# Optimization experiments

Measured on AMD Instinct MI355X. Metric: run time of the kernel, lower is better.

## Reference

```python
import jax, jax.numpy as jnp
import numpy as np
import math

VOCAB = 256
EMBED = 1024
HEADS = 16
MAX_SEQ = 1024
B, S = 4, 1024
EPS = 1e-5


def setup_inputs() -> dict:
    key = jax.random.key(0)
    ks = jax.random.split(key, 10)
    x = jax.random.randint(ks[0], (B, S), 0, VOCAB)
    token_embedding = jax.random.normal(ks[1], (VOCAB, EMBED), dtype=jnp.float32)
    # positional phase buffer: pos * (1/10000**(dim/E)) * pi
    pos = jnp.arange(MAX_SEQ, dtype=jnp.float32)[:, None]
    dim = jnp.arange(EMBED, dtype=jnp.float32)[None, :]
    freq = 1.0 / (10000.0 ** (dim / EMBED))
    pos_phase = pos * freq * math.pi  # [MAX_SEQ, EMBED]
    hd = EMBED // HEADS
    q_rot = jax.random.uniform(ks[2], (HEADS, hd), minval=-math.pi, maxval=math.pi)
    k_rot = jax.random.uniform(ks[3], (HEADS, hd), minval=-math.pi, maxval=math.pi)
    v_rot = jax.random.uniform(ks[4], (HEADS, hd), minval=-math.pi, maxval=math.pi)
    # orthogonal-ish init for ff_real via QR
    a = jax.random.normal(ks[5], (EMBED, EMBED), dtype=jnp.float32)
    ff_real, _ = jnp.linalg.qr(a)
    ff_imag = jax.random.uniform(ks[6], (EMBED, EMBED), minval=-0.01, maxval=0.01)
    lim = 1.0 / math.sqrt(EMBED)
    ro_real_w = jax.random.uniform(ks[7], (VOCAB, EMBED), minval=-lim, maxval=lim)
    ro_real_b = jnp.zeros((VOCAB,), dtype=jnp.float32)
    ro_imag_w = jax.random.uniform(ks[8], (VOCAB, EMBED), minval=-lim, maxval=lim)
    ro_imag_b = jnp.zeros((VOCAB,), dtype=jnp.float32)
    return {
        "x": x,
        "token_embedding": token_embedding,
        "pos_phase": pos_phase,
        "q_rot": q_rot,
        "k_rot": k_rot,
        "v_rot": v_rot,
        "ff_real": ff_real,
        "ff_imag": ff_imag,
        "ro_real_w": ro_real_w,
        "ro_real_b": ro_real_b,
        "ro_imag_w": ro_imag_w,
        "ro_imag_b": ro_imag_b,
    }


def complex_norm(z):
    mag = jnp.abs(z)
    mean_mag = jnp.mean(mag, axis=-1, keepdims=True)
    std_mag = jnp.std(mag, axis=-1, keepdims=True, ddof=1)  # torch std is unbiased
    norm_mag = (mag - mean_mag) / (std_mag + EPS)
    scale = jnp.tanh(norm_mag) / (mag + EPS)
    return z * scale.astype(jnp.complex64)


def reference(x, token_embedding, pos_phase, q_rot, k_rot, v_rot,
              ff_real, ff_imag, ro_real_w, ro_real_b, ro_imag_w, ro_imag_b):
    b, s = x.shape
    h, hd = q_rot.shape
    mag = jnp.tanh(token_embedding[x])                       # [B,S,E]
    state = mag.astype(jnp.complex64) * jnp.exp(1j * pos_phase[:s].astype(jnp.complex64))[None]
    sh = state.reshape(b, s, h, hd)                          # [B,S,H,hd]
    q = sh * jnp.exp(1j * q_rot.astype(jnp.complex64))
    k = sh * jnp.exp(1j * k_rot.astype(jnp.complex64))
    v = sh * jnp.exp(1j * v_rot.astype(jnp.complex64))
    # complex QK^H interference -> take real part as logits
    interference = jnp.einsum('bqhd,bkhd->bhqk', q, jnp.conj(k))
    attn_logits = interference.real / math.sqrt(hd)
    causal = jnp.tril(jnp.ones((s, s), dtype=bool))
    attn_logits = jnp.where(causal[None, None], attn_logits, -jnp.inf)
    attn_weights = jax.nn.softmax(attn_logits * 8.0, axis=-1)  # [B,H,S,S]
    attn_out = jnp.einsum('bhqk,bkhd->bqhd', attn_weights.astype(jnp.complex64), v)
    attn_out = attn_out.reshape(b, s, h * hd)
    state = state + attn_out
    ff = ff_real.astype(jnp.complex64) + 1j * ff_imag.astype(jnp.complex64)
    state = state @ ff
    state = complex_norm(state)
    return state.real @ ro_real_w.T + ro_real_b + state.imag @ ro_imag_w.T + ro_imag_b
```

## Files before the change

### kernel.cpp

```cpp
#include <hip/hip_runtime.h>
#include <math.h>

#define B_ 4
#define S_ 1024
#define E_ 1024
#define H_ 16
#define V_ 256

typedef _Float16 h8 __attribute__((ext_vector_type(8)));
typedef _Float16 h4 __attribute__((ext_vector_type(4)));
typedef float f4x __attribute__((ext_vector_type(4)));

__device__ __forceinline__ void gload16(const void* g, void* l) {
  __builtin_amdgcn_global_load_lds((const __attribute__((address_space(1))) void*)g,
                                   (__attribute__((address_space(3))) void*)l, 16, 0, 0);
}

#define MFMA32F16(a, b, c) __builtin_amdgcn_mfma_f32_16x16x32_f16(a, b, c, 0, 0, 0)

#if defined(__has_builtin)
#if __has_builtin(__builtin_amdgcn_mfma_f32_16x16x16f16)
#define MFMA16F16(a, b, c) __builtin_amdgcn_mfma_f32_16x16x16f16(a, b, c, 0, 0, 0)
#endif
#endif
#ifndef MFMA16F16
__device__ __forceinline__ f4x mfma16f16_asm(h4 a, h4 b, f4x c) {
  asm volatile("v_mfma_f32_16x16x16_f16 %0, %1, %2, %0" : "+v"(c) : "v"(a), "v"(b));
  return c;
}
#define MFMA16F16(a, b, c) mfma16f16_asm(a, b, c)
#endif

__global__ void rot_kernel(const float* __restrict__ qr, const float* __restrict__ kr,
                           const float* __restrict__ vr, float* __restrict__ tabs) {
  int i = blockIdx.x * blockDim.x + threadIdx.x;
  if (i >= 3 * 1024) return;
  int which = i >> 10;
  int j = i & 1023;
  const float* src = which == 0 ? qr : (which == 1 ? kr : vr);
  float s, c;
  sincosf(src[j], &s, &c);
  tabs[which * 2048 + j] = c;
  tabs[which * 2048 + 1024 + j] = s;
}

__global__ __launch_bounds__(256) void embed_qkv_kernel(
    const int* __restrict__ x, const float* __restrict__ te,
    const float* __restrict__ pp, const float* __restrict__ tabs,
    float* __restrict__ sr, float* __restrict__ si,
    unsigned short* __restrict__ Kd, unsigned short* __restrict__ Vd) {
  __shared__ unsigned short Kl2[4096];
  __shared__ unsigned short Vl2[4096];
  const int kt2 = blockIdx.x;
  const int bh = blockIdx.y;
  const int b = bh >> 4, h = bh & 15;
  const int tid = threadIdx.x;
  const float* qc = tabs + h * 64;
  const float* qs = tabs + 1024 + h * 64;
  const float* kc = tabs + 2048 + h * 64;
  const float* ks = tabs + 3072 + h * 64;
  #pragma unroll
  for (int p = 0; p < 8; ++p) {
    int id = p * 256 + tid;
    int sl = id >> 6;
    int dd = id & 63;
    int s = kt2 * 32 + sl;
    int e = h * 64 + dd;
    int tok = x[b * 1024 + s];
    float mm = tanhf(te[tok * 1024 + e]);
    float sn, cs;
    sincosf(pp[s * 1024 + e], &sn, &cs);
    float re = mm * cs, im = mm * sn;
    size_t g = ((size_t)(b * 1024 + s)) * 1024 + e;
    sr[g] = re;
    si[g] = im;
    float cq = qc[dd], sq = qs[dd], ck = kc[dd], sk = ks[dd];
    float cd = cq * ck + sq * sk;
    float sd = sq * ck - cq * sk;
    float kr = re * cd + im * sd;
    float ki = im * cd - re * sd;
    int t = sl >> 4, key = sl & 15;
    int c0 = dd, c1 = 64 + dd;
    #define KOFF(c) (t * 2048 + ((((c) >> 5) * 4 + (((c) >> 3) & 3)) * 16 + key) * 8 + ((c) & 7))
    *(_Float16*)&Kl2[KOFF(c0)] = (_Float16)kr;
    *(_Float16*)&Kl2[KOFF(c1)] = (_Float16)ki;
    #undef KOFF
    int kgk = key >> 2, jk = key & 3;
    #define VOFF(d) (t * 2048 + ((((d) >> 4) * 4 + kgk) * 16 + ((d) & 15)) * 4 + jk)
    *(_Float16*)&Vl2[VOFF(dd)] = (_Float16)re;
    *(_Float16*)&Vl2[VOFF(64 + dd)] = (_Float16)im;
    #undef VOFF
  }
  __syncthreads();
  unsigned short* kdst = Kd + ((size_t)(bh * 64 + kt2 * 2)) * 2048;
  unsigned short* vdst = Vd + ((size_t)(bh * 64 + kt2 * 2)) * 2048;
  #pragma unroll
  for (int p = 0; p < 2; ++p) {
    int c = p * 256 + tid;
    ((int4*)kdst)[c] = ((const int4*)Kl2)[c];
    ((int4*)vdst)[c] = ((const int4*)Vl2)[c];
  }
}

__global__ __launch_bounds__(256, 4) void attn_mfma_kernel(
    const float* __restrict__ sr, const float* __restrict__ si,
    const unsigned short* __restrict__ Kd, const unsigned short* __restrict__ Vd,
    const float* __restrict__ tabs,
    unsigned short* __restrict__ Af) {
  __shared__ __align__(16) unsigned short Klds[2][4096];
  __shared__ __align__(16) unsigned short Vlds[2][4096];
  const int flat = blockIdx.x;
  const int low = flat & 7, rest = flat >> 3;
  const int a = rest >> 3;
  const int bh = ((rest & 7) << 3) | low;
  const int b = bh >> 4, h = bh & 15;
  const int tid = threadIdx.x, lane = tid & 63, wid = tid >> 6;
  const int cl = lane & 15, kg = lane >> 4;
  const int atile = (wid >> 1) ? (31 - a) : a;
  const int qw0 = atile * 32 + (wid & 1) * 16;

  h8 qf[4];
  {
    int q = qw0 + cl;
    const float* srow = sr + ((size_t)(b * 1024 + q)) * 1024 + h * 64;
    const float* irow = si + ((size_t)(b * 1024 + q)) * 1024 + h * 64;
    #pragma unroll
    for (int ksx = 0; ksx < 4; ++ksx) {
      int f0 = ksx * 32 + kg * 8;
      const float* src = (f0 < 64) ? (srow + f0) : (irow + (f0 - 64));
      float4 v0 = *(const float4*)src;
      float4 v1 = *(const float4*)(src + 4);
      qf[ksx][0] = (_Float16)v0.x; qf[ksx][1] = (_Float16)v0.y;
      qf[ksx][2] = (_Float16)v0.z; qf[ksx][3] = (_Float16)v0.w;
      qf[ksx][4] = (_Float16)v1.x; qf[ksx][5] = (_Float16)v1.y;
      qf[ksx][6] = (_Float16)v1.z; qf[ksx][7] = (_Float16)v1.w;
    }
  }

  f4x acc[8] = {};
  float m_ = -1e30f, l_ = 0.f;
  const int np = 32 - a;
  const int wqmax = qw0 + 15;
  const int qcol = qw0 + cl;

  const unsigned short* kstream = Kd + ((size_t)(bh * 64)) * 2048;
  const unsigned short* vstream = Vd + ((size_t)(bh * 64)) * 2048;

  #define STAGE_PAIR(buf, P)                                                    \
    {                                                                           \
      const unsigned short* kb = kstream + (size_t)(P) * 4096;                  \
      const unsigned short* vb = vstream + (size_t)(P) * 4096;                  \
      _Pragma("unroll")                                                         \
      for (int r = 0; r < 2; ++r) {                                             \
        int off = r * 256 + wid * 64;                                           \
        gload16(kb + (size_t)(off + lane) * 8, &Klds[buf][off * 8]);            \
        gload16(vb + (size_t)(off + lane) * 8, &Vlds[buf][off * 8]);            \
      }                                                                         \
    }

  STAGE_PAIR(0, 0)
  __syncthreads();

  for (int p = 0; p < np; ++p) {
    const int cur = p & 1;
    if (p + 1 < np) STAGE_PAIR(cur ^ 1, p + 1)
    const int k0a = p * 32;
    if (k0a <= wqmax) {
      __builtin_amdgcn_s_setprio(1);
      f4x sca = {}, scb = {};
      #pragma unroll
      for (int ksx = 0; ksx < 4; ++ksx) {
        h8 ka = *(const h8*)&Klds[cur][ksx * 512 + lane * 8];
        sca = MFMA32F16(ka, qf[ksx], sca);
      }
      #pragma unroll
      for (int ksx = 0; ksx < 4; ++ksx) {
        h8 kb = *(const h8*)&Klds[cur][2048 + ksx * 512 + lane * 8];
        scb = MFMA32F16(kb, qf[ksx], scb);
      }
      __builtin_amdgcn_s_setprio(0);
      if (k0a + 31 > qw0) {
        #pragma unroll
        for (int r = 0; r < 4; ++r) {
          if (k0a + kg * 4 + r > qcol)      sca[r] = -1e30f;
          if (k0a + 16 + kg * 4 + r > qcol) scb[r] = -1e30f;
        }
      }
      float mx = fmaxf(fmaxf(fmaxf(sca[0], sca[1]), fmaxf(sca[2], sca[3])),
                       fmaxf(fmaxf(scb[0], scb[1]), fmaxf(scb[2], scb[3])));
      mx = fmaxf(mx, __shfl_xor(mx, 16, 64));
      mx = fmaxf(mx, __shfl_xor(mx, 32, 64));
      if (!__all(mx <= m_ + 8.0f)) {
        float mn = fmaxf(m_, mx);
        float corr = __expf(m_ - mn);
        #pragma unroll
        for (int mt = 0; mt < 8; ++mt) acc[mt] *= corr;
        l_ *= corr;
        m_ = mn;
      }
      float pa0 = __expf(sca[0] - m_), pa1 = __expf(sca[1] - m_);
      float pa2 = __expf(sca[2] - m_), pa3 = __expf(sca[3] - m_);
      float pb0 = __expf(scb[0] - m_), pb1 = __expf(scb[1] - m_);
      float pb2 = __expf(scb[2] - m_), pb3 = __expf(scb[3] - m_);
      float s0 = ((pa0 + pa1) + (pa2 + pa3)) + ((pb0 + pb1) + (pb2 + pb3));
      s0 += __shfl_xor(s0, 16, 64);
      s0 += __shfl_xor(s0, 32, 64);
      l_ += s0;
      h4 pba, pbb;
      pba[0] = (_Float16)pa0; pba[1] = (_Float16)pa1;
      pba[2] = (_Float16)pa2; pba[3] = (_Float16)pa3;
      pbb[0] = (_Float16)pb0; pbb[1] = (_Float16)pb1;
      pbb[2] = (_Float16)pb2; pbb[3] = (_Float16)pb3;
      __builtin_amdgcn_s_setprio(1);
      #pragma unroll
      for (int mt = 0; mt < 8; ++mt) {
        h4 va = *(const h4*)&Vlds[cur][mt * 256 + lane * 4];
        acc[mt] = MFMA16F16(va, pba, acc[mt]);
      }
      #pragma unroll
      for (int mt = 0; mt < 8; ++mt) {
        h4 vb = *(const h4*)&Vlds[cur][2048 + mt * 256 + lane * 4];
        acc[mt] = MFMA16F16(vb, pbb, acc[mt]);
      }
      __builtin_amdgcn_s_setprio(0);
    }
    __syncthreads();
  }
  #undef STAGE_PAIR
  {
    float linv = 1.0f / l_;
    int q = qw0 + cl;
    size_t mrow = (size_t)(b * 1024 + q);
    size_t obase = mrow * 1024 + h * 64;
    size_t abase = mrow * 2048 + h * 64;
    #pragma unroll
    for (int mt = 0; mt < 4; ++mt) {
      int d0 = mt * 16 + kg * 4;
      float4 s_r = *(const float4*)&sr[obase + d0];
      float4 s_i = *(const float4*)&si[obase + d0];
      float srv[4] = {s_r.x, s_r.y, s_r.z, s_r.w};
      float siv[4] = {s_i.x, s_i.y, s_i.z, s_i.w};
      h4 hr, hi;
      #pragma unroll
      for (int r = 0; r < 4; ++r) {
        int d = d0 + r;
        float orv = acc[mt][r] * linv;
        float oiv = acc[mt + 4][r] * linv;
        float c = tabs[4096 + h * 64 + d], s = tabs[5120 + h * 64 + d];
        hr[r] = (_Float16)(orv * c - oiv * s + srv[r]);
        hi[r] = (_Float16)(orv * s + oiv * c + siv[r]);
      }
      *(h4*)&Af[abase + d0]        = hr;
      *(h4*)&Af[abase + 1024 + d0] = hi;
    }
  }
}

__global__ void split_b_kernel(const float* __restrict__ fr, const float* __restrict__ fi,
                               unsigned short* __restrict__ Bt) {
  __shared__ float tile[32][33];
  const int k0 = blockIdx.x * 32, n0 = blockIdx.y * 32;
  const int tid = threadIdx.x;
  #pragma unroll
  for (int p = 0; p < 4; ++p) {
    int e = p * 256 + tid;
    int kk = e >> 5, nn = e & 31;
    int k = k0 + kk, n = n0 + nn;
    float v;
    if (n < 1024) v = (k < 1024) ? fr[(size_t)k * 1024 + n] : -fi[(size_t)(k - 1024) * 1024 + n];
    else          v = (k < 1024) ? fi[(size_t)k * 1024 + (n - 1024)]
                                 : fr[(size_t)(k - 1024) * 1024 + (n - 1024)];
    tile[kk][nn] = v;
  }
  __syncthreads();
  #pragma unroll
  for (int p = 0; p < 4; ++p) {
    int e = p * 256 + tid;
    int nn = e >> 5, kk = e & 31;
    *(_Float16*)&Bt[(size_t)(n0 + nn) * 2048 + (k0 + kk)] = (_Float16)tile[kk][nn];
  }
}

__global__ void split_w_kernel(const float* __restrict__ wr, const float* __restrict__ wi,
                               unsigned short* __restrict__ Wt) {
  int idx = blockIdx.x * 256 + threadIdx.x;
  int v = idx >> 9;
  int k4 = (idx & 511) * 4;
  float4 a = (k4 < 1024) ? *(const float4*)&wr[(size_t)v * 1024 + k4]
                         : *(const float4*)&wi[(size_t)v * 1024 + k4 - 1024];
  h4 h;
  h[0] = (_Float16)a.x; h[1] = (_Float16)a.y;
  h[2] = (_Float16)a.z; h[3] = (_Float16)a.w;
  *(h4*)&Wt[(size_t)v * 2048 + k4] = h;
}

__global__ __launch_bounds__(256, 4) void gemm_ff(
    const unsigned short* __restrict__ A,
    const unsigned short* __restrict__ Bt,
    float* __restrict__ pr0, float* __restrict__ pi0,
    float* __restrict__ pr1, float* __restrict__ pi1) {
  __shared__ short As[128 * 64];
  __shared__ short Bs[128 * 64];
  const int tid = threadIdx.x;
  const int lane = tid & 63, wid = tid >> 6;
  const int m0 = blockIdx.x * 128, n0 = blockIdx.y * 128;
  const int z = blockIdx.z;
  const int wr = wid >> 1, wc = wid & 1;
  const int cl = lane & 15, rg = lane >> 4;

  f4x acc[4][4] = {};
  const int cbase = wid * 256;

  for (int kt = z * 16; kt < z * 16 + 16; ++kt) {
    const int k0 = kt * 64;
    #pragma unroll
    for (int it = 0; it < 4; ++it) {
      int c = cbase + it * 64 + lane;
      gload16(A + (size_t)(m0 + (c >> 3)) * 2048 + k0 + (c & 7) * 8,
              As + (cbase + it * 64) * 8);
      gload16(Bt + (size_t)(n0 + (c >> 3)) * 2048 + k0 + (c & 7) * 8,
              Bs + (cbase + it * 64) * 8);
    }
    __syncthreads();
    #pragma unroll
    for (int ks = 0; ks < 2; ++ks) {
      h8 a[4], b[4];
      #pragma unroll
      for (int ms = 0; ms < 4; ++ms)
        a[ms] = *(const h8*)&As[(wr * 64 + ms * 16 + cl) * 64 + ks * 32 + rg * 8];
      #pragma unroll
      for (int ns = 0; ns < 4; ++ns)
        b[ns] = *(const h8*)&Bs[(wc * 64 + ns * 16 + cl) * 64 + ks * 32 + rg * 8];
      #pragma unroll
      for (int ms = 0; ms < 4; ++ms)
        #pragma unroll
        for (int ns = 0; ns < 4; ++ns)
          acc[ms][ns] = MFMA32F16(a[ms], b[ns], acc[ms][ns]);
    }
    __syncthreads();
  }

  const int colbase = n0 + wc * 64;
  float* o_r = z ? pr1 : pr0;
  float* o_i = z ? pi1 : pi0;
  float* dst = (colbase < 1024) ? o_r : o_i;
  const int cb = colbase & 1023;
  #pragma unroll
  for (int ms = 0; ms < 4; ++ms)
    #pragma unroll
    for (int r2 = 0; r2 < 4; ++r2) {
      const int grow = m0 + wr * 64 + ms * 16 + rg * 4 + r2;
      #pragma unroll
      for (int ns = 0; ns < 4; ++ns)
        dst[(size_t)grow * 1024 + cb + ns * 16 + cl] = acc[ms][ns][r2];
    }
}

__global__ __launch_bounds__(256, 4) void gemm_ro(
    const unsigned short* __restrict__ Z,
    const unsigned short* __restrict__ Wt,
    float* __restrict__ part) {
  __shared__ short As[128 * 64];
  __shared__ short Bs[128 * 64];
  const int tid = threadIdx.x;
  const int lane = tid & 63, wid = tid >> 6;
  const int m0 = blockIdx.x * 128, n0 = blockIdx.y * 128;
  const int z = blockIdx.z;
  const int wr = wid >> 1, wc = wid & 1;
  const int cl = lane & 15, rg = lane >> 4;

  f4x acc[4][4] = {};
  const int cbase = wid * 256;

  for (int kt = z * 4; kt < z * 4 + 4; ++kt) {
    const int k0 = kt * 64;
    #pragma unroll
    for (int it = 0; it < 4; ++it) {
      int c = cbase + it * 64 + lane;
      gload16(Z + (size_t)(m0 + (c >> 3)) * 2048 + k0 + (c & 7) * 8,
              As + (cbase + it * 64) * 8);
      gload16(Wt + (size_t)(n0 + (c >> 3)) * 2048 + k0 + (c & 7) * 8,
              Bs + (cbase + it * 64) * 8);
    }
    __syncthreads();
    #pragma unroll
    for (int ks = 0; ks < 2; ++ks) {
      h8 a[4], b[4];
      #pragma unroll
      for (int ms = 0; ms < 4; ++ms)
        a[ms] = *(const h8*)&As[(wr * 64 + ms * 16 + cl) * 64 + ks * 32 + rg * 8];
      #pragma unroll
      for (int ns = 0; ns < 4; ++ns)
        b[ns] = *(const h8*)&Bs[(wc * 64 + ns * 16 + cl) * 64 + ks * 32 + rg * 8];
      #pragma unroll
      for (int ms = 0; ms < 4; ++ms)
        #pragma unroll
        for (int ns = 0; ns < 4; ++ns)
          acc[ms][ns] = MFMA32F16(a[ms], b[ns], acc[ms][ns]);
    }
    __syncthreads();
  }

  float* dst = part + (size_t)z * 4096 * 256;
  const int colbase = n0 + wc * 64;
  #pragma unroll
  for (int ms = 0; ms < 4; ++ms)
    #pragma unroll
    for (int r2 = 0; r2 < 4; ++r2) {
      const int grow = m0 + wr * 64 + ms * 16 + rg * 4 + r2;
      #pragma unroll
      for (int ns = 0; ns < 4; ++ns)
        dst[(size_t)grow * 256 + colbase + ns * 16 + cl] = acc[ms][ns][r2];
    }
}

__global__ __launch_bounds__(256) void norm_split_kernel(
    const float* __restrict__ pr0, const float* __restrict__ pi0,
    const float* __restrict__ pr1, const float* __restrict__ pi1,
    unsigned short* __restrict__ Z) {
  const int row = blockIdx.x, tid = threadIdx.x;
  const int base = row * E_ + tid * 4;
  float4 r0 = *(const float4*)&pr0[base];
  float4 r1 = *(const float4*)&pr1[base];
  float4 i0 = *(const float4*)&pi0[base];
  float4 i1 = *(const float4*)&pi1[base];
  float4 zr = make_float4(r0.x + r1.x, r0.y + r1.y, r0.z + r1.z, r0.w + r1.w);
  float4 zi = make_float4(i0.x + i1.x, i0.y + i1.y, i0.z + i1.z, i0.w + i1.w);
  float mg[4];
  mg[0] = sqrtf(zr.x * zr.x + zi.x * zi.x);
  mg[1] = sqrtf(zr.y * zr.y + zi.y * zi.y);
  mg[2] = sqrtf(zr.z * zr.z + zi.z * zi.z);
  mg[3] = sqrtf(zr.w * zr.w + zi.w * zi.w);
  float s1 = mg[0] + mg[1] + mg[2] + mg[3];
  float s2 = mg[0]*mg[0] + mg[1]*mg[1] + mg[2]*mg[2] + mg[3]*mg[3];
  #pragma unroll
  for (int off = 1; off < 64; off <<= 1) {
    s1 += __shfl_xor(s1, off, 64);
    s2 += __shfl_xor(s2, off, 64);
  }
  __shared__ float ws1[4], ws2[4];
  if ((tid & 63) == 0) { ws1[tid >> 6] = s1; ws2[tid >> 6] = s2; }
  __syncthreads();
  s1 = ws1[0] + ws1[1] + ws1[2] + ws1[3];
  s2 = ws2[0] + ws2[1] + ws2[2] + ws2[3];
  float mean = s1 * (1.0f / 1024.0f);
  float var = (s2 - 1024.0f * mean * mean) * (1.0f / 1023.0f);
  var = fmaxf(var, 0.0f);
  float inv_sd = 1.0f / (sqrtf(var) + 1e-5f);
  float sc[4];
  #pragma unroll
  for (int t = 0; t < 4; ++t)
    sc[t] = tanhf((mg[t] - mean) * inv_sd) / (mg[t] + 1e-5f);
  h4 hr, hi;
  hr[0] = (_Float16)(zr.x * sc[0]); hr[1] = (_Float16)(zr.y * sc[1]);
  hr[2] = (_Float16)(zr.z * sc[2]); hr[3] = (_Float16)(zr.w * sc[3]);
  hi[0] = (_Float16)(zi.x * sc[0]); hi[1] = (_Float16)(zi.y * sc[1]);
  hi[2] = (_Float16)(zi.z * sc[2]); hi[3] = (_Float16)(zi.w * sc[3]);
  const size_t zb = (size_t)row * 2048 + tid * 4;
  *(h4*)&Z[zb]        = hr;
  *(h4*)&Z[zb + 1024] = hi;
}

__global__ void reduce_bias_kernel(const float* __restrict__ part,
                                   const float* __restrict__ rb,
                                   const float* __restrict__ ib,
                                   float* __restrict__ out) {
  int i4 = (blockIdx.x * 256 + threadIdx.x) * 4;
  int col = i4 & 255;
  float4 s = *(const float4*)&part[i4];
  #pragma unroll
  for (int z = 1; z < 8; ++z) {
    float4 v = *(const float4*)&part[(size_t)z * 1048576 + i4];
    s.x += v.x; s.y += v.y; s.z += v.z; s.w += v.w;
  }
  s.x += rb[col + 0] + ib[col + 0];
  s.y += rb[col + 1] + ib[col + 1];
  s.z += rb[col + 2] + ib[col + 2];
  s.w += rb[col + 3] + ib[col + 3];
  *(float4*)&out[i4] = s;
}

extern "C" void kernel_launch(void* const* d_in, const int* in_sizes, int n_in,
                              void* d_out, int out_size, void* d_ws, size_t ws_size,
                              hipStream_t stream) {
  const int*   x    = (const int*)d_in[0];
  const float* te   = (const float*)d_in[1];
  const float* pp   = (const float*)d_in[2];
  const float* qr   = (const float*)d_in[3];
  const float* kr   = (const float*)d_in[4];
  const float* vr   = (const float*)d_in[5];
  const float* ffr  = (const float*)d_in[6];
  const float* ffi  = (const float*)d_in[7];
  const float* rorw = (const float*)d_in[8];
  const float* rorb = (const float*)d_in[9];
  const float* roiw = (const float*)d_in[10];
  const float* roib = (const float*)d_in[11];
  float* out = (float*)d_out;

  char* W = (char*)d_ws;
  const size_t MiB = 1 << 20;
  float* sr  = (float*)W;
  float* si  = (float*)(W + 16 * MiB);
  unsigned short* Af = (unsigned short*)(W + 32 * MiB);
  unsigned short* Kd = (unsigned short*)(W + 48 * MiB);
  unsigned short* Vd = (unsigned short*)(W + 64 * MiB);
  unsigned short* Bt = (unsigned short*)(W + 48 * MiB);
  unsigned short* Wt = (unsigned short*)(W + 56 * MiB);
  float* tabs = (float*)(W + 96 * MiB);
  float* pr0 = sr;
  float* pi0 = si;
  float* pr1 = (float*)(W + 64 * MiB);
  float* pi1 = (float*)(W + 80 * MiB);
  unsigned short* Zhl = Af;
  float* ro_part = (float*)(W + 64 * MiB);

  rot_kernel<<<12, 256, 0, stream>>>(qr, kr, vr, tabs);
  embed_qkv_kernel<<<dim3(32, 64), 256, 0, stream>>>(x, te, pp, tabs, sr, si, Kd, Vd);
  attn_mfma_kernel<<<1024, 256, 0, stream>>>(sr, si, Kd, Vd, tabs, Af);
  split_b_kernel<<<dim3(64, 64), 256, 0, stream>>>(ffr, ffi, Bt);
  split_w_kernel<<<512, 256, 0, stream>>>(rorw, roiw, Wt);
  gemm_ff<<<dim3(32, 16, 2), 256, 0, stream>>>(Af, Bt, pr0, pi0, pr1, pi1);
  norm_split_kernel<<<B_ * S_, 256, 0, stream>>>(pr0, pi0, pr1, pi1, Zhl);
  gemm_ro<<<dim3(32, 2, 8), 256, 0, stream>>>(Zhl, Wt, ro_part);
  reduce_bias_kernel<<<1024, 256, 0, stream>>>(ro_part, rorb, roib, out);
}
```

Measured before the change: 156.0 us.

## Store state in fp16, use fast sincos/tanh, packed converts, XCD-aware GEMM block mapping

The embedding kernel now writes the real and imaginary state as fp16 instead of fp32, which halves the traffic for the attention kernel's Q loads and residual reads. tanhf and sincosf are replaced with an exp-based tanh and hardware v_sin/v_cos on range-reduced revolutions. Softmax probabilities are packed to fp16 with cvt_pkrtz, and both GEMMs remap block indices so neighbouring M tiles land on the same XCD for L2 reuse. These changes trade some accuracy from fp16 state and approximate transcendentals; the gemm_ff remap assumes its grid layout matches gemm_ro's.

```diff
diff --git a/kernel.cpp b/kernel.cpp
--- a/kernel.cpp
+++ b/kernel.cpp
@@ -9,6 +9,7 @@
 
 typedef _Float16 h8 __attribute__((ext_vector_type(8)));
 typedef _Float16 h4 __attribute__((ext_vector_type(4)));
+typedef __fp16 f16x2 __attribute__((ext_vector_type(2)));
 typedef float f4x __attribute__((ext_vector_type(4)));
 
 __device__ __forceinline__ void gload16(const void* g, void* l) {
@@ -30,6 +31,18 @@
 }
 #define MFMA16F16(a, b, c) mfma16f16_asm(a, b, c)
 #endif
+
+__device__ __forceinline__ void fast_sincos(float x, float* s, float* c) {
+  float rev = x * 0.15915494309189535f;
+  rev = rev - floorf(rev);
+  float sv, cv;
+  asm("v_sin_f32 %0, %1" : "=v"(sv) : "v"(rev));
+  asm("v_cos_f32 %0, %1" : "=v"(cv) : "v"(rev));
+  *s = sv; *c = cv;
+}
+__device__ __forceinline__ float fast_tanh(float x) {
+  return 1.0f - 2.0f / (__expf(2.0f * x) + 1.0f);
+}
 
 __global__ void rot_kernel(const float* __restrict__ qr, const float* __restrict__ kr,
                            const float* __restrict__ vr, float* __restrict__ tabs) {
@@ -47,7 +60,7 @@
 __global__ __launch_bounds__(256) void embed_qkv_kernel(
     const int* __restrict__ x, const float* __restrict__ te,
     const float* __restrict__ pp, const float* __restrict__ tabs,
-    float* __restrict__ sr, float* __restrict__ si,
+    unsigned short* __restrict__ srh, unsigned short* __restrict__ sih,
     unsigned short* __restrict__ Kd, unsigned short* __restrict__ Vd) {
   __shared__ unsigned short Kl2[4096];
   __shared__ unsigned short Vl2[4096];
@@ -67,13 +80,13 @@
     int s = kt2 * 32 + sl;
     int e = h * 64 + dd;
     int tok = x[b * 1024 + s];
-    float mm = tanhf(te[tok * 1024 + e]);
+    float mm = fast_tanh(te[tok * 1024 + e]);
     float sn, cs;
-    sincosf(pp[s * 1024 + e], &sn, &cs);
+    fast_sincos(pp[s * 1024 + e], &sn, &cs);
     float re = mm * cs, im = mm * sn;
     size_t g = ((size_t)(b * 1024 + s)) * 1024 + e;
-    sr[g] = re;
-    si[g] = im;
+    *(_Float16*)&srh[g] = (_Float16)re;
+    *(_Float16*)&sih[g] = (_Float16)im;
     float cq = qc[dd], sq = qs[dd], ck = kc[dd], sk = ks[dd];
     float cd = cq * ck + sq * sk;
     float sd = sq * ck - cq * sk;
@@ -103,7 +116,7 @@
 }
 
 __global__ __launch_bounds__(256, 4) void attn_mfma_kernel(
-    const float* __restrict__ sr, const float* __restrict__ si,
+    const unsigned short* __restrict__ srh, const unsigned short* __restrict__ sih,
     const unsigned short* __restrict__ Kd, const unsigned short* __restrict__ Vd,
     const float* __restrict__ tabs,
     unsigned short* __restrict__ Af) {
@@ -122,18 +135,12 @@
   h8 qf[4];
   {
     int q = qw0 + cl;
-    const float* srow = sr + ((size_t)(b * 1024 + q)) * 1024 + h * 64;
-    const float* irow = si + ((size_t)(b * 1024 + q)) * 1024 + h * 64;
+    const unsigned short* srow = srh + ((size_t)(b * 1024 + q)) * 1024 + h * 64;
+    const unsigned short* irow = sih + ((size_t)(b * 1024 + q)) * 1024 + h * 64;
     #pragma unroll
     for (int ksx = 0; ksx < 4; ++ksx) {
       int f0 = ksx * 32 + kg * 8;
-      const float* src = (f0 < 64) ? (srow + f0) : (irow + (f0 - 64));
-      float4 v0 = *(const float4*)src;
-      float4 v1 = *(const float4*)(src + 4);
-      qf[ksx][0] = (_Float16)v0.x; qf[ksx][1] = (_Float16)v0.y;
-      qf[ksx][2] = (_Float16)v0.z; qf[ksx][3] = (_Float16)v0.w;
-      qf[ksx][4] = (_Float16)v1.x; qf[ksx][5] = (_Float16)v1.y;
-      qf[ksx][6] = (_Float16)v1.z; qf[ksx][7] = (_Float16)v1.w;
+      qf[ksx] = (f0 < 64) ? *(const h8*)(srow + f0) : *(const h8*)(irow + (f0 - 64));
     }
   }
 
@@ -206,11 +213,15 @@
       s0 += __shfl_xor(s0, 16, 64);
       s0 += __shfl_xor(s0, 32, 64);
       l_ += s0;
+      f16x2 a01 = __builtin_amdgcn_cvt_pkrtz(pa0, pa1);
+      f16x2 a23 = __builtin_amdgcn_cvt_pkrtz(pa2, pa3);
+      f16x2 b01 = __builtin_amdgcn_cvt_pkrtz(pb0, pb1);
+      f16x2 b23 = __builtin_amdgcn_cvt_pkrtz(pb2, pb3);
       h4 pba, pbb;
-      pba[0] = (_Float16)pa0; pba[1] = (_Float16)pa1;
-      pba[2] = (_Float16)pa2; pba[3] = (_Float16)pa3;
-      pbb[0] = (_Float16)pb0; pbb[1] = (_Float16)pb1;
-      pbb[2] = (_Float16)pb2; pbb[3] = (_Float16)pb3;
+      pba[0] = (_Float16)a01[0]; pba[1] = (_Float16)a01[1];
+      pba[2] = (_Float16)a23[0]; pba[3] = (_Float16)a23[1];
+      pbb[0] = (_Float16)b01[0]; pbb[1] = (_Float16)b01[1];
+      pbb[2] = (_Float16)b23[0]; pbb[3] = (_Float16)b23[1];
       __builtin_amdgcn_s_setprio(1);
       #pragma unroll
       for (int mt = 0; mt < 8; ++mt) {
@@ -236,10 +247,8 @@
     #pragma unroll
     for (int mt = 0; mt < 4; ++mt) {
       int d0 = mt * 16 + kg * 4;
-      float4 s_r = *(const float4*)&sr[obase + d0];
-      float4 s_i = *(const float4*)&si[obase + d0];
-      float srv[4] = {s_r.x, s_r.y, s_r.z, s_r.w};
-      float siv[4] = {s_i.x, s_i.y, s_i.z, s_i.w};
+      h4 s_r = *(const h4*)&srh[obase + d0];
+      h4 s_i = *(const h4*)&sih[obase + d0];
       h4 hr, hi;
       #pragma unroll
       for (int r = 0; r < 4; ++r) {
@@ -247,8 +256,8 @@
         float orv = acc[mt][r] * linv;
         float oiv = acc[mt + 4][r] * linv;
         float c = tabs[4096 + h * 64 + d], s = tabs[5120 + h * 64 + d];
-        hr[r] = (_Float16)(orv * c - oiv * s + srv[r]);
-        hi[r] = (_Float16)(orv * s + oiv * c + siv[r]);
+        hr[r] = (_Float16)(orv * c - oiv * s + (float)s_r[r]);
+        hi[r] = (_Float16)(orv * s + oiv * c + (float)s_i[r]);
       }
       *(h4*)&Af[abase + d0]        = hr;
       *(h4*)&Af[abase + 1024 + d0] = hi;
@@ -303,7 +312,10 @@
   __shared__ short Bs[128 * 64];
   const int tid = threadIdx.x;
   const int lane = tid & 63, wid = tid >> 6;
-  const int m0 = blockIdx.x * 128, n0 = blockIdx.y * 128;
+  const int l = blockIdx.x + (blockIdx.y << 5);
+  const int xcd = l & 7, j = l >> 3;
+  const int m0 = ((xcd << 2) + (j & 3)) << 7;
+  const int n0 = (j >> 2) << 7;
   const int z = blockIdx.z;
   const int wr = wid >> 1, wc = wid & 1;
   const int cl = lane & 15, rg = lane >> 4;
@@ -364,7 +376,10 @@
   __shared__ short Bs[128 * 64];
   const int tid = threadIdx.x;
   const int lane = tid & 63, wid = tid >> 6;
-  const int m0 = blockIdx.x * 128, n0 = blockIdx.y * 128;
+  const int l = blockIdx.x + (blockIdx.y << 5);
+  const int xcd = l & 7, j = l >> 3;
+  const int m0 = ((xcd << 2) + (j & 3)) << 7;
+  const int n0 = (j >> 2) << 7;
   const int z = blockIdx.z;
   const int wr = wid >> 1, wc = wid & 1;
   const int cl = lane & 15, rg = lane >> 4;
@@ -499,24 +514,24 @@
 
   char* W = (char*)d_ws;
   const size_t MiB = 1 << 20;
-  float* sr  = (float*)W;
-  float* si  = (float*)(W + 16 * MiB);
+  unsigned short* srh = (unsigned short*)W;
+  unsigned short* sih = (unsigned short*)(W + 16 * MiB);
   unsigned short* Af = (unsigned short*)(W + 32 * MiB);
   unsigned short* Kd = (unsigned short*)(W + 48 * MiB);
   unsigned short* Vd = (unsigned short*)(W + 64 * MiB);
   unsigned short* Bt = (unsigned short*)(W + 48 * MiB);
   unsigned short* Wt = (unsigned short*)(W + 56 * MiB);
   float* tabs = (float*)(W + 96 * MiB);
-  float* pr0 = sr;
-  float* pi0 = si;
+  float* pr0 = (float*)W;
+  float* pi0 = (float*)(W + 16 * MiB);
   float* pr1 = (float*)(W + 64 * MiB);
   float* pi1 = (float*)(W + 80 * MiB);
   unsigned short* Zhl = Af;
   float* ro_part = (float*)(W + 64 * MiB);
 
   rot_kernel<<<12, 256, 0, stream>>>(qr, kr, vr, tabs);
-  embed_qkv_kernel<<<dim3(32, 64), 256, 0, stream>>>(x, te, pp, tabs, sr, si, Kd, Vd);
-  attn_mfma_kernel<<<1024, 256, 0, stream>>>(sr, si, Kd, Vd, tabs, Af);
+  embed_qkv_kernel<<<dim3(32, 64), 256, 0, stream>>>(x, te, pp, tabs, srh, sih, Kd, Vd);
+  attn_mfma_kernel<<<1024, 256, 0, stream>>>(srh, sih, Kd, Vd, tabs, Af);
   split_b_kernel<<<dim3(64, 64), 256, 0, stream>>>(ffr, ffi, Bt);
   split_w_kernel<<<512, 256, 0, stream>>>(rorw, roiw, Wt);
   gemm_ff<<<dim3(32, 16, 2), 256, 0, stream>>>(Af, Bt, pr0, pi0, pr1, pi1);
```

Result: faster. 148.5 us (-4.8%).
